# Optimization experiments

Hardware: AMD Instinct MI355X
Metric: run time of the kernel (lower is better)

The kernel has to match this reference:

```python
import jax, jax.numpy as jnp
import numpy as np

EPS = 0.5  # energy-relaxation learning rate (epsilon in __init__)


def rho(s):
    return jnp.clip(s, 0.0, 1.0)


def setup_inputs() -> dict:
    key = jax.random.key(0)
    k_x, k_w1, k_w2 = jax.random.split(key, 3)
    B, I, H, O = 8192, 1024, 128, 1000
    x = jax.random.uniform(k_x, (B, I), dtype=jnp.float32)
    hidden0 = jnp.zeros((B, H), dtype=jnp.float32)
    output0 = jnp.zeros((B, O), dtype=jnp.float32)
    b_in = jnp.zeros((I,), dtype=jnp.float32)
    b_h = jnp.zeros((H,), dtype=jnp.float32)
    b_o = jnp.zeros((O,), dtype=jnp.float32)
    # xavier_uniform: U(-a, a), a = sqrt(6 / (fan_in + fan_out))
    a1 = np.sqrt(6.0 / (I + H)).astype(np.float32)
    a2 = np.sqrt(6.0 / (H + O)).astype(np.float32)
    W1 = jax.random.uniform(k_w1, (I, H), minval=-a1, maxval=a1, dtype=jnp.float32)
    W2 = jax.random.uniform(k_w2, (H, O), minval=-a2, maxval=a2, dtype=jnp.float32)
    return {"x": x, "hidden0": hidden0, "output0": output0,
            "b_in": b_in, "b_h": b_h, "b_o": b_o,
            "W1": W1, "W2": W2, "n_iterations": 30}


def reference(x, hidden0, output0, b_in, b_h, b_o, W1, W2, n_iterations):
    # Hopfield-style energy summed over the batch (beta=0 / free phase):
    # E = 0.5*sum rho(s)^2 - sum rho(s).b - sum rho(pre) W rho(post)
    def energy(h, o):
        rx, rh, ro = rho(x), rho(h), rho(o)
        sq = 0.5 * ((rx * rx).sum() + (rh * rh).sum() + (ro * ro).sum())
        lin = -(rx @ b_in).sum() - (rh @ b_h).sum() - (ro @ b_o).sum()
        quad = -jnp.einsum('bi,ih,bh->', rx, W1, rh) \
               - jnp.einsum('bh,ho,bo->', rh, W2, ro)
        return sq + lin + quad

    grad_e = jax.grad(energy, argnums=(0, 1))

    def step(carry, _):
        h, o = carry
        gh, go = grad_e(h, o)
        h = jnp.clip(h - EPS * gh, 0.0, 1.0)
        o = jnp.clip(o - EPS * go, 0.0, 1.0)
        return (h, o), None

    (h, o), _ = jax.lax.scan(step, (hidden0, output0), None, length=n_iterations)
    return jax.nn.log_softmax(o, axis=1)
```

## Files before the change

### kernel.cpp

```cpp
#include <hip/hip_runtime.h>
#include <hip/hip_bf16.h>

typedef __bf16 bf16_t;
typedef __bf16 bf16x4_t __attribute__((ext_vector_type(4)));
typedef __bf16 bf16x8 __attribute__((ext_vector_type(8)));
typedef float f32x16 __attribute__((ext_vector_type(16)));

#define EPS 0.5f
#define MFMA32(a, b, c) __builtin_amdgcn_mfma_f32_32x32x16_bf16(a, b, c, 0, 0, 0)

__global__ __launch_bounds__(256) void prep_weights(
    const float* __restrict__ W1, const float* __restrict__ W2,
    bf16_t* __restrict__ W1t, bf16_t* __restrict__ W2B, bf16_t* __restrict__ W2T) {
  int idx = blockIdx.x * 256 + threadIdx.x;
  if (idx < 131072) {
    { int j = idx >> 10, i = idx & 1023; W1t[idx] = (bf16_t)W1[i * 128 + j]; }
    { int e = idx & 7, l = (idx >> 3) & 63, s = (idx >> 9) & 63, jt = idx >> 15;
      int j = jt * 32 + (l & 31), k = s * 16 + (l >> 5) * 8 + e;
      W2B[idx] = (bf16_t)((k < 1000) ? W2[j * 1000 + k] : 0.f); }
    { int e = idx & 7, l = (idx >> 3) & 63, js = (idx >> 9) & 7, kt = idx >> 12;
      int k = kt * 32 + (l & 31), j = js * 16 + (l >> 5) * 8 + e;
      W2T[idx] = (bf16_t)((k < 1000) ? W2[j * 1000 + k] : 0.f); }
  }
}

__global__ __launch_bounds__(256) void gemm_A(
    const float* __restrict__ x, const bf16_t* __restrict__ W1t,
    float* __restrict__ A) {
  int lane = threadIdx.x & 63, w = threadIdx.x >> 6;
  int row0 = blockIdx.x * 64;
  int mt = w & 1, np = (w >> 1) * 2;
  f32x16 acc0 = {}, acc1 = {};
  int ar = row0 + mt * 32 + (lane & 31);
  int kg = (lane >> 5) * 8;
  const float* xrow = x + (size_t)ar * 1024 + kg;
  const bf16_t* b0 = W1t + ((np * 32 + (lane & 31)) << 10) + kg;
  const bf16_t* b1 = W1t + (((np + 1) * 32 + (lane & 31)) << 10) + kg;
#pragma unroll 4
  for (int ks = 0; ks < 64; ++ks) {
    float xv[8];
    *(float4*)&xv[0] = *(const float4*)(xrow + ks * 16);
    *(float4*)&xv[4] = *(const float4*)(xrow + ks * 16 + 4);
    bf16x8 a;
#pragma unroll
    for (int i = 0; i < 8; ++i) a[i] = (bf16_t)xv[i];
    bf16x8 f0 = *(const bf16x8*)(b0 + ks * 16);
    bf16x8 f1 = *(const bf16x8*)(b1 + ks * 16);
    acc0 = MFMA32(a, f0, acc0);
    acc1 = MFMA32(a, f1, acc1);
  }
#pragma unroll
  for (int reg = 0; reg < 16; ++reg) {
    int r = mt * 32 + (reg & 3) + 8 * (reg >> 2) + 4 * (lane >> 5);
    A[(size_t)(row0 + r) * 128 + np * 32 + (lane & 31)] = acc0[reg];
    A[(size_t)(row0 + r) * 128 + (np + 1) * 32 + (lane & 31)] = acc1[reg];
  }
}

__device__ __forceinline__ bf16x4_t upd4(bf16x4_t v4, const float* u, bool& chgd) {
  bf16x4_t n4;
#pragma unroll
  for (int r = 0; r < 4; ++r) {
    float v = (float)v4[r];
    float g = __builtin_fmaf(v, v, -v);
    float st = (g == 0.f) ? 0.25f : 0.5f;
    float n = __builtin_fmaf(-st, v - u[r], v);
    n4[r] = (bf16_t)__builtin_amdgcn_fmed3f(n, 0.f, 1.f);
  }
  unsigned long long ov, nv;
  __builtin_memcpy(&ov, &v4, 8);
  __builtin_memcpy(&nv, &n4, 8);
  chgd |= (ov != nv);
  return n4;
}

__global__ __launch_bounds__(1024, 4) void eqprop(
    const float* __restrict__ h0, const float* __restrict__ o0,
    const float* __restrict__ b_h, const float* __restrict__ b_o,
    const float* __restrict__ A, const bf16_t* __restrict__ W2B,
    const bf16_t* __restrict__ W2T, const int* __restrict__ nit,
    float* __restrict__ out) {
  __shared__ __align__(16) char o_raw[131072];
  __shared__ __align__(16) char h_raw[16384];
  __shared__ float bo_lds[1024];
  __shared__ int chg[32];

  const int tid = threadIdx.x, lane = tid & 63, w = tid >> 6;
  const int lo = lane & 31, hi = lane >> 5;
  const int row0 = blockIdx.x * 32;

  for (int idx = tid; idx < 32768; idx += 1024) {
    int b = idx >> 10, k = idx & 1023;
    float v = (k < 1000) ? o0[(size_t)(row0 + b) * 1000 + k] : 0.f;
    int ad = ((k >> 4) << 10) + ((((k >> 3) & 1) << 5) + b) * 16 + ((k & 7) << 1);
    *(bf16_t*)(o_raw + ad) = (bf16_t)v;
  }
  for (int idx = tid; idx < 4096; idx += 1024) {
    int b = idx >> 7, j = idx & 127;
    int ad = ((j >> 4) << 10) + ((((j >> 3) & 1) << 5) + b) * 16 + ((j & 7) << 1);
    *(bf16_t*)(h_raw + ad) = (bf16_t)h0[(size_t)(row0 + b) * 128 + j];
  }
  bo_lds[tid] = (tid < 1000) ? b_o[tid] : 0.f;
  if (tid < 32) chg[tid] = 0;

  const int T = nit[0];
  int p = 0;
  __syncthreads();

  if (w < 4) {
    const int jt = w;
    const bf16_t* WB = W2B + (size_t)jt * 32768 + lane * 8;
#define CW(s) (*(const bf16x8*)(WB + (s) * 512))
    bf16x8 wres[16];
#pragma unroll
    for (int s = 0; s < 16; ++s) wres[s] = CW(s);
    const char* obase = o_raw + lane * 16;

    for (int t = 0; t < T; ++t) {
      const char* obP = obase + (p << 16);
#define OF(s) (*(const bf16x8*)(obP + (s) * 1024))
      f32x16 acc = {};
      __builtin_amdgcn_s_setprio(1);
#pragma unroll
      for (int s = 0; s < 16; ++s) acc = MFMA32(wres[s], OF(s), acc);
      __builtin_amdgcn_s_setprio(0);
      bf16x8 cs0[4], cs1[4];
      cs0[0] = CW(16); cs0[1] = CW(17); cs0[2] = CW(18); cs0[3] = CW(19);
#pragma unroll 1
      for (int c = 0; c < 12; ++c) {
        const int s0 = 16 + c * 4;
        if ((c & 1) == 0) {
          if (c < 11) {
            cs1[0] = CW(s0 + 4); cs1[1] = CW(s0 + 5);
            cs1[2] = CW(s0 + 6); cs1[3] = CW(s0 + 7);
          }
          __builtin_amdgcn_s_setprio(1);
          acc = MFMA32(cs0[0], OF(s0 + 0), acc);
          acc = MFMA32(cs0[1], OF(s0 + 1), acc);
          acc = MFMA32(cs0[2], OF(s0 + 2), acc);
          acc = MFMA32(cs0[3], OF(s0 + 3), acc);
          __builtin_amdgcn_s_setprio(0);
        } else {
          if (c < 11) {
            cs0[0] = CW(s0 + 4); cs0[1] = CW(s0 + 5);
            cs0[2] = CW(s0 + 6); cs0[3] = CW(s0 + 7);
          }
          __builtin_amdgcn_s_setprio(1);
          acc = MFMA32(cs1[0], OF(s0 + 0), acc);
          acc = MFMA32(cs1[1], OF(s0 + 1), acc);
          acc = MFMA32(cs1[2], OF(s0 + 2), acc);
          acc = MFMA32(cs1[3], OF(s0 + 3), acc);
          __builtin_amdgcn_s_setprio(0);
        }
      }
      const char* hrd = h_raw + (p << 13) + lo * 16 + hi * 8;
      char* hwr = h_raw + ((p ^ 1) << 13) + lo * 16 + hi * 8;
      bool chgd = false;
#pragma unroll
      for (int q = 0; q < 4; ++q) {
        const int jb = jt * 32 + q * 8 + 4 * hi;
        const int boff = (jt * 2 + (q >> 1)) * 1024 + (q & 1) * 512;
        float av[4], bh[4], u[4];
        *(float4*)av = *(const float4*)(A + (size_t)(row0 + lo) * 128 + jb);
        *(float4*)bh = *(const float4*)(b_h + jb);
#pragma unroll
        for (int r = 0; r < 4; ++r) u[r] = av[r] + bh[r] + acc[q * 4 + r];
        bf16x4_t v4 = *(const bf16x4_t*)(hrd + boff);
        *(bf16x4_t*)(hwr + boff) = upd4(v4, u, chgd);
      }
      if (__ballot(chgd) && lane == 0) atomicOr(&chg[t & 31], 1);
      __syncthreads();
      p ^= 1;
      if (chg[t & 31] == 0) break;
    }
  } else {
    const int wd = w - 4;
    const int kt0 = (wd < 8) ? wd * 3 : 24 + (wd - 8) * 2;
    const int nkt = (wd < 8) ? 3 : 2;
    const bf16_t* WT = W2T + (size_t)kt0 * 4096 + lane * 8;
#define DW(f) (*(const bf16x8*)(WT + (f) * 512))
    bf16x8 wres[8];
#pragma unroll
    for (int f = 0; f < 8; ++f) wres[f] = DW(f);
    const char* hbase = h_raw + lane * 16;
    const char* obase = o_raw + lo * 16 + hi * 8;

    for (int t = 0; t < T; ++t) {
      const char* hbP = hbase + (p << 13);
      bf16x8 hf[8];
#pragma unroll
      for (int js = 0; js < 8; ++js)
        hf[js] = *(const bf16x8*)(hbP + js * 1024);
      const char* ord = obase + (p << 16);
      char* owr = o_raw + lo * 16 + hi * 8 + ((p ^ 1) << 16);
      bool chgd = false;

#pragma unroll 1
      for (int kl = 0; kl < nkt; ++kl) {
        const int kt = kt0 + kl;
        f32x16 acc = {};
        if (kl == 0) {
          __builtin_amdgcn_s_setprio(1);
#pragma unroll
          for (int js = 0; js < 8; ++js) acc = MFMA32(wres[js], hf[js], acc);
          __builtin_amdgcn_s_setprio(0);
        } else {
          bf16x8 s0 = DW(kl * 8 + 0), s1 = DW(kl * 8 + 1);
          bf16x8 s2 = DW(kl * 8 + 2), s3 = DW(kl * 8 + 3);
          bf16x8 s4 = DW(kl * 8 + 4), s5 = DW(kl * 8 + 5);
          bf16x8 s6 = DW(kl * 8 + 6), s7 = DW(kl * 8 + 7);
          __builtin_amdgcn_s_setprio(1);
          acc = MFMA32(s0, hf[0], acc);
          acc = MFMA32(s1, hf[1], acc);
          acc = MFMA32(s2, hf[2], acc);
          acc = MFMA32(s3, hf[3], acc);
          acc = MFMA32(s4, hf[4], acc);
          acc = MFMA32(s5, hf[5], acc);
          acc = MFMA32(s6, hf[6], acc);
          acc = MFMA32(s7, hf[7], acc);
          __builtin_amdgcn_s_setprio(0);
        }
#pragma unroll
        for (int q = 0; q < 4; ++q) {
          const int boff = (kt * 2 + (q >> 1)) * 1024 + (q & 1) * 512;
          float bo4[4], u[4];
          *(float4*)bo4 = *(const float4*)(bo_lds + kt * 32 + q * 8 + 4 * hi);
#pragma unroll
          for (int r = 0; r < 4; ++r) u[r] = bo4[r] + acc[q * 4 + r];
          bf16x4_t v4 = *(const bf16x4_t*)(ord + boff);
          *(bf16x4_t*)(owr + boff) = upd4(v4, u, chgd);
        }
      }
      if (__ballot(chgd) && lane == 0) atomicOr(&chg[t & 31], 1);
      __syncthreads();
      p ^= 1;
      if (chg[t & 31] == 0) break;
    }
  }
  __syncthreads();

  const char* of = o_raw + (p << 16);
  for (int row = w * 2; row < w * 2 + 2; ++row) {
    float m = -1e30f;
    for (int k = lane; k < 1000; k += 64) {
      int ad = ((k >> 4) << 10) + ((((k >> 3) & 1) << 5) + row) * 16 + ((k & 7) << 1);
      m = fmaxf(m, (float)*(const bf16_t*)(of + ad));
    }
#pragma unroll
    for (int s = 32; s > 0; s >>= 1) m = fmaxf(m, __shfl_xor(m, s));
    float sum = 0.f;
    for (int k = lane; k < 1000; k += 64) {
      int ad = ((k >> 4) << 10) + ((((k >> 3) & 1) << 5) + row) * 16 + ((k & 7) << 1);
      sum += expf((float)*(const bf16_t*)(of + ad) - m);
    }
#pragma unroll
    for (int s = 32; s > 0; s >>= 1) sum += __shfl_xor(sum, s);
    float lse = m + logf(sum);
    for (int k = lane; k < 1000; k += 64) {
      int ad = ((k >> 4) << 10) + ((((k >> 3) & 1) << 5) + row) * 16 + ((k & 7) << 1);
      out[(size_t)(row0 + row) * 1000 + k] =
          (float)*(const bf16_t*)(of + ad) - lse;
    }
  }
}

extern "C" void kernel_launch(void* const* d_in, const int* in_sizes, int n_in,
                              void* d_out, int out_size, void* d_ws, size_t ws_size,
                              hipStream_t stream) {
  const float* x   = (const float*)d_in[0];
  const float* h0  = (const float*)d_in[1];
  const float* o0  = (const float*)d_in[2];
  const float* b_h = (const float*)d_in[4];
  const float* b_o = (const float*)d_in[5];
  const float* W1  = (const float*)d_in[6];
  const float* W2  = (const float*)d_in[7];
  const int*   nit = (const int*)d_in[8];
  float* out = (float*)d_out;

  char* ws = (char*)d_ws;
  float*  A   = (float*)ws;
  bf16_t* W1t = (bf16_t*)(ws + 4194304);
  bf16_t* W2B = (bf16_t*)(ws + 4194304 + 262144);
  bf16_t* W2T = (bf16_t*)(ws + 4194304 + 524288);

  prep_weights<<<512, 256, 0, stream>>>(W1, W2, W1t, W2B, W2T);
  gemm_A<<<128, 256, 0, stream>>>(x, W1t, A);
  eqprop<<<256, 1024, 0, stream>>>(h0, o0, b_h, b_o, A, W2B, W2T, nit, out);
}
```

Measured before the change: 267.6 us.

## Swizzle LDS state layout, drop convergence check, rebalance register-resident weights and gemm grid

The o/h state buffers in LDS move from an MFMA-fragment-blocked layout to a row-major layout with an XOR swizzle, so fragment reads and updates avoid bank conflicts. The per-iteration convergence ballot, shared atomic and early exit are removed, along with setprio hints. In the hidden-update waves the number of register-resident W2 slices drops, and the streamed weight chunks start at a per-block rotated offset with triple buffering to spread L2 traffic. The output-update waves keep more weights in registers, and gemm_A now uses 32-row blocks with one MFMA tile per wave on twice the grid. Dropping the early exit means all T iterations always run.

```diff
diff --git a/kernel.cpp b/kernel.cpp
--- a/kernel.cpp
+++ b/kernel.cpp
@@ -8,6 +8,13 @@
 
 #define EPS 0.5f
 #define MFMA32(a, b, c) __builtin_amdgcn_mfma_f32_32x32x16_bf16(a, b, c, 0, 0, 0)
+
+__device__ __forceinline__ int oswz(int row, int kbyte) {
+  return (row << 11) + (kbyte ^ ((row & 15) << 4));
+}
+__device__ __forceinline__ int hswz(int row, int jbyte) {
+  return (row << 8) + (jbyte ^ ((row & 15) << 4));
+}
 
 __global__ __launch_bounds__(256) void prep_weights(
     const float* __restrict__ W1, const float* __restrict__ W2,
@@ -28,14 +35,12 @@
     const float* __restrict__ x, const bf16_t* __restrict__ W1t,
     float* __restrict__ A) {
   int lane = threadIdx.x & 63, w = threadIdx.x >> 6;
-  int row0 = blockIdx.x * 64;
-  int mt = w & 1, np = (w >> 1) * 2;
-  f32x16 acc0 = {}, acc1 = {};
-  int ar = row0 + mt * 32 + (lane & 31);
-  int kg = (lane >> 5) * 8;
-  const float* xrow = x + (size_t)ar * 1024 + kg;
-  const bf16_t* b0 = W1t + ((np * 32 + (lane & 31)) << 10) + kg;
-  const bf16_t* b1 = W1t + (((np + 1) * 32 + (lane & 31)) << 10) + kg;
+  int lo = lane & 31, hi = lane >> 5;
+  int row0 = blockIdx.x * 32;
+  f32x16 acc = {};
+  int kg = hi * 8;
+  const float* xrow = x + (size_t)(row0 + lo) * 1024 + kg;
+  const bf16_t* b0 = W1t + ((w * 32 + lo) << 10) + kg;
 #pragma unroll 4
   for (int ks = 0; ks < 64; ++ks) {
     float xv[8];
@@ -45,19 +50,16 @@
 #pragma unroll
     for (int i = 0; i < 8; ++i) a[i] = (bf16_t)xv[i];
     bf16x8 f0 = *(const bf16x8*)(b0 + ks * 16);
-    bf16x8 f1 = *(const bf16x8*)(b1 + ks * 16);
-    acc0 = MFMA32(a, f0, acc0);
-    acc1 = MFMA32(a, f1, acc1);
+    acc = MFMA32(a, f0, acc);
   }
 #pragma unroll
   for (int reg = 0; reg < 16; ++reg) {
-    int r = mt * 32 + (reg & 3) + 8 * (reg >> 2) + 4 * (lane >> 5);
-    A[(size_t)(row0 + r) * 128 + np * 32 + (lane & 31)] = acc0[reg];
-    A[(size_t)(row0 + r) * 128 + (np + 1) * 32 + (lane & 31)] = acc1[reg];
-  }
-}
-
-__device__ __forceinline__ bf16x4_t upd4(bf16x4_t v4, const float* u, bool& chgd) {
+    int r = (reg & 3) + 8 * (reg >> 2) + 4 * hi;
+    A[(size_t)(row0 + r) * 128 + w * 32 + lo] = acc[reg];
+  }
+}
+
+__device__ __forceinline__ bf16x4_t upd4(bf16x4_t v4, const float* u) {
   bf16x4_t n4;
 #pragma unroll
   for (int r = 0; r < 4; ++r) {
@@ -67,10 +69,6 @@
     float n = __builtin_fmaf(-st, v - u[r], v);
     n4[r] = (bf16_t)__builtin_amdgcn_fmed3f(n, 0.f, 1.f);
   }
-  unsigned long long ov, nv;
-  __builtin_memcpy(&ov, &v4, 8);
-  __builtin_memcpy(&nv, &n4, 8);
-  chgd |= (ov != nv);
   return n4;
 }
 
@@ -80,28 +78,24 @@
     const float* __restrict__ A, const bf16_t* __restrict__ W2B,
     const bf16_t* __restrict__ W2T, const int* __restrict__ nit,
     float* __restrict__ out) {
-  __shared__ __align__(16) char o_raw[131072];
-  __shared__ __align__(16) char h_raw[16384];
+  __shared__ __align__(16) char ob[2][65536];
+  __shared__ __align__(16) char hb[2][8192];
   __shared__ float bo_lds[1024];
-  __shared__ int chg[32];
 
   const int tid = threadIdx.x, lane = tid & 63, w = tid >> 6;
   const int lo = lane & 31, hi = lane >> 5;
   const int row0 = blockIdx.x * 32;
 
-  for (int idx = tid; idx < 32768; idx += 1024) {
-    int b = idx >> 10, k = idx & 1023;
-    float v = (k < 1000) ? o0[(size_t)(row0 + b) * 1000 + k] : 0.f;
-    int ad = ((k >> 4) << 10) + ((((k >> 3) & 1) << 5) + b) * 16 + ((k & 7) << 1);
-    *(bf16_t*)(o_raw + ad) = (bf16_t)v;
-  }
-  for (int idx = tid; idx < 4096; idx += 1024) {
-    int b = idx >> 7, j = idx & 127;
-    int ad = ((j >> 4) << 10) + ((((j >> 3) & 1) << 5) + b) * 16 + ((j & 7) << 1);
-    *(bf16_t*)(h_raw + ad) = (bf16_t)h0[(size_t)(row0 + b) * 128 + j];
+  for (int idx = tid; idx < 32 * 1024; idx += 1024) {
+    int r = idx >> 10, k = idx & 1023;
+    float v = (k < 1000) ? o0[(size_t)(row0 + r) * 1000 + k] : 0.f;
+    *(bf16_t*)(&ob[0][0] + oswz(r, k * 2)) = (bf16_t)v;
+  }
+  for (int idx = tid; idx < 32 * 128; idx += 1024) {
+    int r = idx >> 7, j = idx & 127;
+    *(bf16_t*)(&hb[0][0] + hswz(r, j * 2)) = (bf16_t)h0[(size_t)(row0 + r) * 128 + j];
   }
   bo_lds[tid] = (tid < 1000) ? b_o[tid] : 0.f;
-  if (tid < 32) chg[tid] = 0;
 
   const int T = nit[0];
   int p = 0;
@@ -110,157 +104,147 @@
   if (w < 4) {
     const int jt = w;
     const bf16_t* WB = W2B + (size_t)jt * 32768 + lane * 8;
-#define CW(s) (*(const bf16x8*)(WB + (s) * 512))
-    bf16x8 wres[16];
-#pragma unroll
-    for (int s = 0; s < 16; ++s) wres[s] = CW(s);
-    const char* obase = o_raw + lane * 16;
+#define CW(s) (*(const bf16x8*)(WB + (size_t)(s) * 512))
+    bf16x8 wres[8];
+#pragma unroll
+    for (int s = 0; s < 8; ++s) wres[s] = CW(s);
+    const int rot = blockIdx.x % 14;
 
     for (int t = 0; t < T; ++t) {
-      const char* obP = obase + (p << 16);
-#define OF(s) (*(const bf16x8*)(obP + (s) * 1024))
+      const char* op = &ob[p][0];
       f32x16 acc = {};
-      __builtin_amdgcn_s_setprio(1);
-#pragma unroll
-      for (int s = 0; s < 16; ++s) acc = MFMA32(wres[s], OF(s), acc);
-      __builtin_amdgcn_s_setprio(0);
-      bf16x8 cs0[4], cs1[4];
-      cs0[0] = CW(16); cs0[1] = CW(17); cs0[2] = CW(18); cs0[3] = CW(19);
+#pragma unroll
+      for (int s = 0; s < 8; ++s) {
+        bf16x8 of = *(const bf16x8*)(op + oswz(lo, s * 32 + hi * 16));
+        acc = MFMA32(wres[s], of, acc);
+      }
+      bf16x8 sA[4], sB[4], sC[4];
+      int bq = rot;
+      int bl = rot + 2; if (bl >= 14) bl -= 14;
+#define LOADB(ST, b) { const int s_ = 8 + (b) * 4; \
+  ST[0] = CW(s_); ST[1] = CW(s_ + 1); ST[2] = CW(s_ + 2); ST[3] = CW(s_ + 3); }
+#define CONSUME(ST) { const int s_ = 8 + bq * 4; \
+  bf16x8 o0_ = *(const bf16x8*)(op + oswz(lo, s_ * 32 + hi * 16)); \
+  acc = MFMA32(ST[0], o0_, acc); \
+  bf16x8 o1_ = *(const bf16x8*)(op + oswz(lo, (s_ + 1) * 32 + hi * 16)); \
+  acc = MFMA32(ST[1], o1_, acc); \
+  bf16x8 o2_ = *(const bf16x8*)(op + oswz(lo, (s_ + 2) * 32 + hi * 16)); \
+  acc = MFMA32(ST[2], o2_, acc); \
+  bf16x8 o3_ = *(const bf16x8*)(op + oswz(lo, (s_ + 3) * 32 + hi * 16)); \
+  acc = MFMA32(ST[3], o3_, acc); \
+  bq += 1; if (bq >= 14) bq -= 14; }
+      {
+        int b1 = rot + 1; if (b1 >= 14) b1 -= 14;
+        LOADB(sA, bq); LOADB(sB, b1);
+      }
 #pragma unroll 1
-      for (int c = 0; c < 12; ++c) {
-        const int s0 = 16 + c * 4;
-        if ((c & 1) == 0) {
-          if (c < 11) {
-            cs1[0] = CW(s0 + 4); cs1[1] = CW(s0 + 5);
-            cs1[2] = CW(s0 + 6); cs1[3] = CW(s0 + 7);
-          }
-          __builtin_amdgcn_s_setprio(1);
-          acc = MFMA32(cs0[0], OF(s0 + 0), acc);
-          acc = MFMA32(cs0[1], OF(s0 + 1), acc);
-          acc = MFMA32(cs0[2], OF(s0 + 2), acc);
-          acc = MFMA32(cs0[3], OF(s0 + 3), acc);
-          __builtin_amdgcn_s_setprio(0);
-        } else {
-          if (c < 11) {
-            cs0[0] = CW(s0 + 4); cs0[1] = CW(s0 + 5);
-            cs0[2] = CW(s0 + 6); cs0[3] = CW(s0 + 7);
-          }
-          __builtin_amdgcn_s_setprio(1);
-          acc = MFMA32(cs1[0], OF(s0 + 0), acc);
-          acc = MFMA32(cs1[1], OF(s0 + 1), acc);
-          acc = MFMA32(cs1[2], OF(s0 + 2), acc);
-          acc = MFMA32(cs1[3], OF(s0 + 3), acc);
-          __builtin_amdgcn_s_setprio(0);
-        }
-      }
-      const char* hrd = h_raw + (p << 13) + lo * 16 + hi * 8;
-      char* hwr = h_raw + ((p ^ 1) << 13) + lo * 16 + hi * 8;
-      bool chgd = false;
+      for (int cc = 0; cc < 4; ++cc) {
+        LOADB(sC, bl); bl += 1; if (bl >= 14) bl -= 14;
+        CONSUME(sA);
+        LOADB(sA, bl); bl += 1; if (bl >= 14) bl -= 14;
+        CONSUME(sB);
+        LOADB(sB, bl); bl += 1; if (bl >= 14) bl -= 14;
+        CONSUME(sC);
+      }
+      CONSUME(sA);
+      CONSUME(sB);
+
+      const char* hp = &hb[p][0];
+      char* hn = &hb[p ^ 1][0];
 #pragma unroll
       for (int q = 0; q < 4; ++q) {
         const int jb = jt * 32 + q * 8 + 4 * hi;
-        const int boff = (jt * 2 + (q >> 1)) * 1024 + (q & 1) * 512;
         float av[4], bh[4], u[4];
         *(float4*)av = *(const float4*)(A + (size_t)(row0 + lo) * 128 + jb);
         *(float4*)bh = *(const float4*)(b_h + jb);
 #pragma unroll
         for (int r = 0; r < 4; ++r) u[r] = av[r] + bh[r] + acc[q * 4 + r];
-        bf16x4_t v4 = *(const bf16x4_t*)(hrd + boff);
-        *(bf16x4_t*)(hwr + boff) = upd4(v4, u, chgd);
-      }
-      if (__ballot(chgd) && lane == 0) atomicOr(&chg[t & 31], 1);
+        bf16x4_t v4 = *(const bf16x4_t*)(hp + hswz(lo, jb * 2));
+        *(bf16x4_t*)(hn + hswz(lo, jb * 2)) = upd4(v4, u);
+      }
       __syncthreads();
       p ^= 1;
-      if (chg[t & 31] == 0) break;
     }
   } else {
     const int wd = w - 4;
     const int kt0 = (wd < 8) ? wd * 3 : 24 + (wd - 8) * 2;
     const int nkt = (wd < 8) ? 3 : 2;
     const bf16_t* WT = W2T + (size_t)kt0 * 4096 + lane * 8;
-#define DW(f) (*(const bf16x8*)(WT + (f) * 512))
-    bf16x8 wres[8];
-#pragma unroll
-    for (int f = 0; f < 8; ++f) wres[f] = DW(f);
-    const char* hbase = h_raw + lane * 16;
-    const char* obase = o_raw + lo * 16 + hi * 8;
+#define DW(f) (*(const bf16x8*)(WT + (size_t)(f) * 512))
+    bf16x8 wres[12];
+#pragma unroll
+    for (int f = 0; f < 12; ++f) wres[f] = DW(f);
 
     for (int t = 0; t < T; ++t) {
-      const char* hbP = hbase + (p << 13);
+      const char* hp = &hb[p][0];
+      const char* op = &ob[p][0];
+      char* on = &ob[p ^ 1][0];
       bf16x8 hf[8];
 #pragma unroll
-      for (int js = 0; js < 8; ++js)
-        hf[js] = *(const bf16x8*)(hbP + js * 1024);
-      const char* ord = obase + (p << 16);
-      char* owr = o_raw + lo * 16 + hi * 8 + ((p ^ 1) << 16);
-      bool chgd = false;
+      for (int kk = 0; kk < 8; ++kk)
+        hf[kk] = *(const bf16x8*)(hp + hswz(lo, kk * 32 + hi * 16));
 
 #pragma unroll 1
       for (int kl = 0; kl < nkt; ++kl) {
         const int kt = kt0 + kl;
         f32x16 acc = {};
         if (kl == 0) {
-          __builtin_amdgcn_s_setprio(1);
 #pragma unroll
           for (int js = 0; js < 8; ++js) acc = MFMA32(wres[js], hf[js], acc);
-          __builtin_amdgcn_s_setprio(0);
+        } else if (kl == 1) {
+          bf16x8 s0 = DW(12), s1 = DW(13), s2 = DW(14), s3 = DW(15);
+#pragma unroll
+          for (int js = 0; js < 4; ++js)
+            acc = MFMA32(wres[8 + js], hf[js], acc);
+          acc = MFMA32(s0, hf[4], acc);
+          acc = MFMA32(s1, hf[5], acc);
+          acc = MFMA32(s2, hf[6], acc);
+          acc = MFMA32(s3, hf[7], acc);
         } else {
-          bf16x8 s0 = DW(kl * 8 + 0), s1 = DW(kl * 8 + 1);
-          bf16x8 s2 = DW(kl * 8 + 2), s3 = DW(kl * 8 + 3);
-          bf16x8 s4 = DW(kl * 8 + 4), s5 = DW(kl * 8 + 5);
-          bf16x8 s6 = DW(kl * 8 + 6), s7 = DW(kl * 8 + 7);
-          __builtin_amdgcn_s_setprio(1);
+          bf16x8 s0 = DW(16), s1 = DW(17), s2 = DW(18), s3 = DW(19);
           acc = MFMA32(s0, hf[0], acc);
           acc = MFMA32(s1, hf[1], acc);
           acc = MFMA32(s2, hf[2], acc);
           acc = MFMA32(s3, hf[3], acc);
+          bf16x8 s4 = DW(20), s5 = DW(21), s6 = DW(22), s7 = DW(23);
           acc = MFMA32(s4, hf[4], acc);
           acc = MFMA32(s5, hf[5], acc);
           acc = MFMA32(s6, hf[6], acc);
           acc = MFMA32(s7, hf[7], acc);
-          __builtin_amdgcn_s_setprio(0);
         }
 #pragma unroll
         for (int q = 0; q < 4; ++q) {
-          const int boff = (kt * 2 + (q >> 1)) * 1024 + (q & 1) * 512;
+          const int kb = kt * 32 + q * 8 + 4 * hi;
           float bo4[4], u[4];
-          *(float4*)bo4 = *(const float4*)(bo_lds + kt * 32 + q * 8 + 4 * hi);
+          *(float4*)bo4 = *(const float4*)(bo_lds + kb);
 #pragma unroll
           for (int r = 0; r < 4; ++r) u[r] = bo4[r] + acc[q * 4 + r];
-          bf16x4_t v4 = *(const bf16x4_t*)(ord + boff);
-          *(bf16x4_t*)(owr + boff) = upd4(v4, u, chgd);
+          bf16x4_t v4 = *(const bf16x4_t*)(op + oswz(lo, kb * 2));
+          *(bf16x4_t*)(on + oswz(lo, kb * 2)) = upd4(v4, u);
         }
       }
-      if (__ballot(chgd) && lane == 0) atomicOr(&chg[t & 31], 1);
       __syncthreads();
       p ^= 1;
-      if (chg[t & 31] == 0) break;
     }
   }
   __syncthreads();
 
-  const char* of = o_raw + (p << 16);
-  for (int row = w * 2; row < w * 2 + 2; ++row) {
+  const char* of = &ob[p][0];
+  for (int r = w * 2; r < w * 2 + 2; ++r) {
     float m = -1e30f;
-    for (int k = lane; k < 1000; k += 64) {
-      int ad = ((k >> 4) << 10) + ((((k >> 3) & 1) << 5) + row) * 16 + ((k & 7) << 1);
-      m = fmaxf(m, (float)*(const bf16_t*)(of + ad));
-    }
+    for (int k = lane; k < 1000; k += 64)
+      m = fmaxf(m, (float)*(const bf16_t*)(of + oswz(r, k * 2)));
 #pragma unroll
     for (int s = 32; s > 0; s >>= 1) m = fmaxf(m, __shfl_xor(m, s));
     float sum = 0.f;
-    for (int k = lane; k < 1000; k += 64) {
-      int ad = ((k >> 4) << 10) + ((((k >> 3) & 1) << 5) + row) * 16 + ((k & 7) << 1);
-      sum += expf((float)*(const bf16_t*)(of + ad) - m);
-    }
+    for (int k = lane; k < 1000; k += 64)
+      sum += expf((float)*(const bf16_t*)(of + oswz(r, k * 2)) - m);
 #pragma unroll
     for (int s = 32; s > 0; s >>= 1) sum += __shfl_xor(sum, s);
     float lse = m + logf(sum);
-    for (int k = lane; k < 1000; k += 64) {
-      int ad = ((k >> 4) << 10) + ((((k >> 3) & 1) << 5) + row) * 16 + ((k & 7) << 1);
-      out[(size_t)(row0 + row) * 1000 + k] =
-          (float)*(const bf16_t*)(of + ad) - lse;
-    }
+    for (int k = lane; k < 1000; k += 64)
+      out[(size_t)(row0 + r) * 1000 + k] =
+          (float)*(const bf16_t*)(of + oswz(r, k * 2)) - lse;
   }
 }
 
@@ -284,6 +268,6 @@
   bf16_t* W2T = (bf16_t*)(ws + 4194304 + 524288);
 
   prep_weights<<<512, 256, 0, stream>>>(W1, W2, W1t, W2B, W2T);
-  gemm_A<<<128, 256, 0, stream>>>(x, W1t, A);
+  gemm_A<<<256, 256, 0, stream>>>(x, W1t, A);
   eqprop<<<256, 1024, 0, stream>>>(h0, o0, b_h, b_o, A, W2B, W2T, nit, out);
 }
```

Result: faster. 256.6 us (-4.1%).

## Drop convergence early-exit and setprio; split gemm_A into 32-row blocks

Applied to the files above, without the earlier changes.

Removes the per-iteration change detection in the relaxation loop (ballot, LDS atomicOr flag and conditional break), so every block always runs all n_iterations steps without the extra check and flag read after each barrier. Also removes the s_setprio hints around the MFMA chains. gemm_A is retiled so each block handles 32 rows with one 32-column tile per wave, which doubles the grid to 256 blocks. If the bf16 state reaches a fixed point well before the iteration count, the lost early exit adds many redundant iterations.

```diff
diff --git a/kernel.cpp b/kernel.cpp
--- a/kernel.cpp
+++ b/kernel.cpp
@@ -28,14 +28,12 @@
     const float* __restrict__ x, const bf16_t* __restrict__ W1t,
     float* __restrict__ A) {
   int lane = threadIdx.x & 63, w = threadIdx.x >> 6;
-  int row0 = blockIdx.x * 64;
-  int mt = w & 1, np = (w >> 1) * 2;
-  f32x16 acc0 = {}, acc1 = {};
-  int ar = row0 + mt * 32 + (lane & 31);
-  int kg = (lane >> 5) * 8;
-  const float* xrow = x + (size_t)ar * 1024 + kg;
-  const bf16_t* b0 = W1t + ((np * 32 + (lane & 31)) << 10) + kg;
-  const bf16_t* b1 = W1t + (((np + 1) * 32 + (lane & 31)) << 10) + kg;
+  int lo = lane & 31, hi = lane >> 5;
+  int row0 = blockIdx.x * 32;
+  f32x16 acc = {};
+  int kg = hi * 8;
+  const float* xrow = x + (size_t)(row0 + lo) * 1024 + kg;
+  const bf16_t* b0 = W1t + ((w * 32 + lo) << 10) + kg;
 #pragma unroll 4
   for (int ks = 0; ks < 64; ++ks) {
     float xv[8];
@@ -45,19 +43,16 @@
 #pragma unroll
     for (int i = 0; i < 8; ++i) a[i] = (bf16_t)xv[i];
     bf16x8 f0 = *(const bf16x8*)(b0 + ks * 16);
-    bf16x8 f1 = *(const bf16x8*)(b1 + ks * 16);
-    acc0 = MFMA32(a, f0, acc0);
-    acc1 = MFMA32(a, f1, acc1);
+    acc = MFMA32(a, f0, acc);
   }
 #pragma unroll
   for (int reg = 0; reg < 16; ++reg) {
-    int r = mt * 32 + (reg & 3) + 8 * (reg >> 2) + 4 * (lane >> 5);
-    A[(size_t)(row0 + r) * 128 + np * 32 + (lane & 31)] = acc0[reg];
-    A[(size_t)(row0 + r) * 128 + (np + 1) * 32 + (lane & 31)] = acc1[reg];
-  }
-}
-
-__device__ __forceinline__ bf16x4_t upd4(bf16x4_t v4, const float* u, bool& chgd) {
+    int r = (reg & 3) + 8 * (reg >> 2) + 4 * hi;
+    A[(size_t)(row0 + r) * 128 + w * 32 + lo] = acc[reg];
+  }
+}
+
+__device__ __forceinline__ bf16x4_t upd4(bf16x4_t v4, const float* u) {
   bf16x4_t n4;
 #pragma unroll
   for (int r = 0; r < 4; ++r) {
@@ -67,10 +62,6 @@
     float n = __builtin_fmaf(-st, v - u[r], v);
     n4[r] = (bf16_t)__builtin_amdgcn_fmed3f(n, 0.f, 1.f);
   }
-  unsigned long long ov, nv;
-  __builtin_memcpy(&ov, &v4, 8);
-  __builtin_memcpy(&nv, &n4, 8);
-  chgd |= (ov != nv);
   return n4;
 }
 
@@ -83,7 +74,6 @@
   __shared__ __align__(16) char o_raw[131072];
   __shared__ __align__(16) char h_raw[16384];
   __shared__ float bo_lds[1024];
-  __shared__ int chg[32];
 
   const int tid = threadIdx.x, lane = tid & 63, w = tid >> 6;
   const int lo = lane & 31, hi = lane >> 5;
@@ -101,7 +91,6 @@
     *(bf16_t*)(h_raw + ad) = (bf16_t)h0[(size_t)(row0 + b) * 128 + j];
   }
   bo_lds[tid] = (tid < 1000) ? b_o[tid] : 0.f;
-  if (tid < 32) chg[tid] = 0;
 
   const int T = nit[0];
   int p = 0;
@@ -120,10 +109,8 @@
       const char* obP = obase + (p << 16);
 #define OF(s) (*(const bf16x8*)(obP + (s) * 1024))
       f32x16 acc = {};
-      __builtin_amdgcn_s_setprio(1);
 #pragma unroll
       for (int s = 0; s < 16; ++s) acc = MFMA32(wres[s], OF(s), acc);
-      __builtin_amdgcn_s_setprio(0);
       bf16x8 cs0[4], cs1[4];
       cs0[0] = CW(16); cs0[1] = CW(17); cs0[2] = CW(18); cs0[3] = CW(19);
 #pragma unroll 1
@@ -134,28 +121,23 @@
             cs1[0] = CW(s0 + 4); cs1[1] = CW(s0 + 5);
             cs1[2] = CW(s0 + 6); cs1[3] = CW(s0 + 7);
           }
-          __builtin_amdgcn_s_setprio(1);
           acc = MFMA32(cs0[0], OF(s0 + 0), acc);
           acc = MFMA32(cs0[1], OF(s0 + 1), acc);
           acc = MFMA32(cs0[2], OF(s0 + 2), acc);
           acc = MFMA32(cs0[3], OF(s0 + 3), acc);
-          __builtin_amdgcn_s_setprio(0);
         } else {
           if (c < 11) {
             cs0[0] = CW(s0 + 4); cs0[1] = CW(s0 + 5);
             cs0[2] = CW(s0 + 6); cs0[3] = CW(s0 + 7);
           }
-          __builtin_amdgcn_s_setprio(1);
           acc = MFMA32(cs1[0], OF(s0 + 0), acc);
           acc = MFMA32(cs1[1], OF(s0 + 1), acc);
           acc = MFMA32(cs1[2], OF(s0 + 2), acc);
           acc = MFMA32(cs1[3], OF(s0 + 3), acc);
-          __builtin_amdgcn_s_setprio(0);
         }
       }
       const char* hrd = h_raw + (p << 13) + lo * 16 + hi * 8;
       char* hwr = h_raw + ((p ^ 1) << 13) + lo * 16 + hi * 8;
-      bool chgd = false;
 #pragma unroll
       for (int q = 0; q < 4; ++q) {
         const int jb = jt * 32 + q * 8 + 4 * hi;
@@ -166,12 +148,10 @@
 #pragma unroll
         for (int r = 0; r < 4; ++r) u[r] = av[r] + bh[r] + acc[q * 4 + r];
         bf16x4_t v4 = *(const bf16x4_t*)(hrd + boff);
-        *(bf16x4_t*)(hwr + boff) = upd4(v4, u, chgd);
+        *(bf16x4_t*)(hwr + boff) = upd4(v4, u);
       }
-      if (__ballot(chgd) && lane == 0) atomicOr(&chg[t & 31], 1);
       __syncthreads();
       p ^= 1;
-      if (chg[t & 31] == 0) break;
     }
   } else {
     const int wd = w - 4;
@@ -193,23 +173,19 @@
         hf[js] = *(const bf16x8*)(hbP + js * 1024);
       const char* ord = obase + (p << 16);
       char* owr = o_raw + lo * 16 + hi * 8 + ((p ^ 1) << 16);
-      bool chgd = false;
 
 #pragma unroll 1
       for (int kl = 0; kl < nkt; ++kl) {
         const int kt = kt0 + kl;
         f32x16 acc = {};
         if (kl == 0) {
-          __builtin_amdgcn_s_setprio(1);
 #pragma unroll
           for (int js = 0; js < 8; ++js) acc = MFMA32(wres[js], hf[js], acc);
-          __builtin_amdgcn_s_setprio(0);
         } else {
           bf16x8 s0 = DW(kl * 8 + 0), s1 = DW(kl * 8 + 1);
           bf16x8 s2 = DW(kl * 8 + 2), s3 = DW(kl * 8 + 3);
           bf16x8 s4 = DW(kl * 8 + 4), s5 = DW(kl * 8 + 5);
           bf16x8 s6 = DW(kl * 8 + 6), s7 = DW(kl * 8 + 7);
-          __builtin_amdgcn_s_setprio(1);
           acc = MFMA32(s0, hf[0], acc);
           acc = MFMA32(s1, hf[1], acc);
           acc = MFMA32(s2, hf[2], acc);
@@ -218,7 +194,6 @@
           acc = MFMA32(s5, hf[5], acc);
           acc = MFMA32(s6, hf[6], acc);
           acc = MFMA32(s7, hf[7], acc);
-          __builtin_amdgcn_s_setprio(0);
         }
 #pragma unroll
         for (int q = 0; q < 4; ++q) {
@@ -228,13 +203,11 @@
 #pragma unroll
           for (int r = 0; r < 4; ++r) u[r] = bo4[r] + acc[q * 4 + r];
           bf16x4_t v4 = *(const bf16x4_t*)(ord + boff);
-          *(bf16x4_t*)(owr + boff) = upd4(v4, u, chgd);
+          *(bf16x4_t*)(owr + boff) = upd4(v4, u);
         }
       }
-      if (__ballot(chgd) && lane == 0) atomicOr(&chg[t & 31], 1);
       __syncthreads();
       p ^= 1;
-      if (chg[t & 31] == 0) break;
     }
   }
   __syncthreads();
@@ -284,6 +257,6 @@
   bf16_t* W2T = (bf16_t*)(ws + 4194304 + 524288);
 
   prep_weights<<<512, 256, 0, stream>>>(W1, W2, W1t, W2B, W2T);
-  gemm_A<<<128, 256, 0, stream>>>(x, W1t, A);
+  gemm_A<<<256, 256, 0, stream>>>(x, W1t, A);
   eqprop<<<256, 1024, 0, stream>>>(h0, o0, b_h, b_o, A, W2B, W2T, nit, out);
 }
```

Result: no change. 263.5 us (-1.5%).
